# Optimization experiments

Hardware: AMD Instinct MI355X
Metric: run time of the kernel (lower is better)

## Reference

```python
import jax, jax.numpy as jnp
import numpy as np


def setup_inputs() -> dict:
    key = jax.random.key(0)
    k1, k2, k3 = jax.random.split(key, 3)
    bs, nvars, T, input_dim = 8, 16, 512, 256
    embed_dim, num_embed, codebook_num = 128, 512, 4
    inp = jax.random.normal(k1, (bs, nvars, T, input_dim), dtype=jnp.float32)
    # xavier_normal_ for (input_dim, embed_dim): std = sqrt(2/(fan_in+fan_out))
    xavier_std = float(np.sqrt(2.0 / (input_dim + embed_dim)))
    projector = jax.random.normal(k2, (input_dim, embed_dim), dtype=jnp.float32) * xavier_std
    codebook = jax.random.normal(k3, (codebook_num, num_embed, embed_dim), dtype=jnp.float32)
    return {"input": inp, "projector": projector, "codebook": codebook}


def reference(input, projector, codebook):
    # project: [b,n,t,input_dim] @ [input_dim,embed_dim] -> [b,n,t,d]
    x = jnp.matmul(input, projector)
    # L2-normalize along last dim (matches torch .norm(dim=-1,keepdim=True) division)
    x = x / jnp.linalg.norm(x, axis=-1, keepdims=True)
    cb = codebook / jnp.linalg.norm(codebook, axis=-1, keepdims=True)
    # cosine similarity: [b,n,t,c,m]
    similarity = jnp.einsum('bntd,cmd->bntcm', x, cb)
    # nearest code per codebook: [b,n,t,c]
    idx = jnp.argmax(similarity, axis=-1)
    return idx
```

## Files before the change

kernel.cpp:

```cpp
#include <hip/hip_runtime.h>
#include <math.h>

#define DIN    256
#define DEMB   128
#define NCB    4
#define MCODES 512
#define NCODE  2048
#define MARGIN 1.5e-4f

using bf16x8 = __attribute__((ext_vector_type(8))) short;
using f32x16 = __attribute__((ext_vector_type(16))) float;

static __device__ __forceinline__ unsigned short f2bf(float f) {
    unsigned u = __float_as_uint(f);
    u += 0x7FFFu + ((u >> 16) & 1u);
    return (unsigned short)(u >> 16);
}
static __device__ __forceinline__ float bf2f(unsigned short h) {
    return __uint_as_float(((unsigned)h) << 16);
}
static __device__ __forceinline__ float4 ld4(const float* p) {
    return *reinterpret_cast<const float4*>(p);
}
static __device__ __forceinline__ void gload_lds16(const void* g, void* l) {
    __builtin_amdgcn_global_load_lds(
        (const __attribute__((address_space(1))) void*)g,
        (__attribute__((address_space(3))) void*)l, 16, 0, 0);
}

__global__ __launch_bounds__(256) void prep_codebook(
        const float* __restrict__ cb, float* __restrict__ cbn,
        unsigned short* __restrict__ cbA) {
    const int w = threadIdx.x >> 6, lane = threadIdx.x & 63;
    const int code = blockIdx.x * 4 + w;
    const float2 v = reinterpret_cast<const float2*>(cb + (size_t)code * DEMB)[lane];
    float ss = v.x * v.x + v.y * v.y;
#pragma unroll
    for (int m = 1; m < 64; m <<= 1) ss += __shfl_xor(ss, m, 64);
    const float rn = 1.0f / sqrtf(ss);
    const float x0 = v.x * rn, x1 = v.y * rn;
    reinterpret_cast<float2*>(cbn + (size_t)code * DEMB)[lane] = make_float2(x0, x1);

    const unsigned short h0 = f2bf(x0), h1 = f2bf(x1);
    const unsigned short l0 = f2bf(x0 - bf2f(h0)), l1 = f2bf(x1 - bf2f(h1));
    const int ct = code >> 5, ci = code & 31;
    const int kt = lane >> 3, g = (lane >> 2) & 1, i = 2 * (lane & 3);
    const size_t base = ((size_t)ct * 1024 + kt * 128 + g * 32 + ci) * 8 + i;
    *reinterpret_cast<ushort2*>(cbA + base)       = make_ushort2(h0, h1);
    *reinterpret_cast<ushort2*>(cbA + base + 512) = make_ushort2(l0, l1);
}

__global__ __launch_bounds__(256) void prep_proj(
        const float* __restrict__ proj, unsigned short* __restrict__ pjA) {
    const int t = blockIdx.x * 256 + threadIdx.x;
    const int ci = t & 31, g = (t >> 5) & 1, kt = (t >> 6) & 15, mt = t >> 10;
    const int m = mt * 32 + ci;
    const size_t base = ((size_t)(mt * 16 + kt) * 3) * 512 + (size_t)(g * 32 + ci) * 8;
#pragma unroll
    for (int i = 0; i < 8; ++i) {
        const float v = proj[(size_t)(kt * 16 + g * 8 + i) * DEMB + m];
        const unsigned short h = f2bf(v);
        const float r1 = v - bf2f(h);
        const unsigned short md = f2bf(r1);
        const float r2 = r1 - bf2f(md);
        pjA[base + i]        = h;
        pjA[base + 512 + i]  = md;
        pjA[base + 1024 + i] = f2bf(r2);
    }
}

__global__ __launch_bounds__(256) void project_mfma(
        const float* __restrict__ inp, const unsigned short* __restrict__ pjA,
        float* __restrict__ xw, float* __restrict__ rnw) {
    const int tid = threadIdx.x;
    const int lane = tid & 63, wv = tid >> 6, kg = lane >> 5;
    const int row = blockIdx.x * 128 + wv * 32 + (lane & 31);
    const float* xr = inp + (size_t)row * DIN;
    const unsigned short* pL = pjA + (size_t)lane * 8;

    auto ldin = [&](float4& a, float4& b, int kt) {
        a = ld4(xr + kt * 16 + kg * 8);
        b = ld4(xr + kt * 16 + kg * 8 + 4);
    };

    f32x16 accP[4], accQ[4];
#pragma unroll
    for (int mt = 0; mt < 4; ++mt)
#pragma unroll
        for (int r = 0; r < 16; ++r) { accP[mt][r] = 0.0f; accQ[mt][r] = 0.0f; }

    auto do_step = [&](const float4& c0, const float4& c1, int kt) {
        const float xs[8] = {c0.x, c0.y, c0.z, c0.w, c1.x, c1.y, c1.z, c1.w};
        bf16x8 Bh, Bm, Bl;
#pragma unroll
        for (int e = 0; e < 8; ++e) {
            const float v = xs[e];
            const unsigned short h = f2bf(v);
            const float r1 = v - bf2f(h);
            const unsigned short md = f2bf(r1);
            const float r2 = r1 - bf2f(md);
            Bh[e] = (short)h; Bm[e] = (short)md; Bl[e] = (short)f2bf(r2);
        }
#pragma unroll
        for (int mt = 0; mt < 4; ++mt) {
            const unsigned short* pf = pL + ((size_t)(mt * 16 + kt) * 3) * 512;
            const bf16x8 Ah = *reinterpret_cast<const bf16x8*>(pf);
            const bf16x8 Am = *reinterpret_cast<const bf16x8*>(pf + 512);
            const bf16x8 Al = *reinterpret_cast<const bf16x8*>(pf + 1024);
            accP[mt] = __builtin_amdgcn_mfma_f32_32x32x16_bf16(Ah, Bh, accP[mt], 0, 0, 0);
            accQ[mt] = __builtin_amdgcn_mfma_f32_32x32x16_bf16(Ah, Bm, accQ[mt], 0, 0, 0);
            accQ[mt] = __builtin_amdgcn_mfma_f32_32x32x16_bf16(Am, Bh, accQ[mt], 0, 0, 0);
            accQ[mt] = __builtin_amdgcn_mfma_f32_32x32x16_bf16(Ah, Bl, accQ[mt], 0, 0, 0);
            accQ[mt] = __builtin_amdgcn_mfma_f32_32x32x16_bf16(Al, Bh, accQ[mt], 0, 0, 0);
            accQ[mt] = __builtin_amdgcn_mfma_f32_32x32x16_bf16(Am, Bm, accQ[mt], 0, 0, 0);
        }
    };

    float4 nA0, nA1, nB0, nB1;
    ldin(nA0, nA1, 0);
#pragma unroll 1
    for (int kt = 0; kt < 16; kt += 2) {
        ldin(nB0, nB1, kt + 1);
        do_step(nA0, nA1, kt);
        if (kt + 2 < 16) ldin(nA0, nA1, kt + 2);
        do_step(nB0, nB1, kt + 1);
    }

    float ss = 0.0f;
#pragma unroll
    for (int mt = 0; mt < 4; ++mt)
#pragma unroll
        for (int q = 0; q < 4; ++q) {
            float4 v;
            v.x = accP[mt][q * 4 + 0] + accQ[mt][q * 4 + 0];
            v.y = accP[mt][q * 4 + 1] + accQ[mt][q * 4 + 1];
            v.z = accP[mt][q * 4 + 2] + accQ[mt][q * 4 + 2];
            v.w = accP[mt][q * 4 + 3] + accQ[mt][q * 4 + 3];
            ss += v.x * v.x + v.y * v.y + v.z * v.z + v.w * v.w;
            *reinterpret_cast<float4*>(xw + (size_t)row * DEMB + mt * 32 + q * 8 + kg * 4) = v;
        }
    ss += __shfl_xor(ss, 32, 64);
    if (lane < 32) rnw[row] = 1.0f / sqrtf(ss);
}

__global__ __launch_bounds__(256) void project_kernel(
        const float* __restrict__ inp, const float* __restrict__ proj,
        float* __restrict__ xw, float* __restrict__ rnw) {
    const int tid = threadIdx.x, tx = tid & 31, ty = tid >> 5;
    const int rowBase = blockIdx.x * 64;

    float acc1[8][4];
#pragma unroll
    for (int i = 0; i < 8; ++i)
#pragma unroll
        for (int j = 0; j < 4; ++j) acc1[i][j] = 0.0f;

    const float* inRow0 = inp + (size_t)(rowBase + ty) * DIN;
    const float* pjCol  = proj + tx * 4;

    float4 ivA[8], ivB[8], pjA[4], pjB[4];
    auto load_step = [&](float4 iv[8], float4 pj[4], int kk) {
#pragma unroll
        for (int j = 0; j < 4; ++j) pj[j] = ld4(pjCol + (size_t)(kk + j) * DEMB);
#pragma unroll
        for (int i = 0; i < 8; ++i) iv[i] = ld4(inRow0 + (size_t)(8 * i) * DIN + kk);
    };
    auto fma_step = [&](const float4 iv[8], const float4 pj[4]) {
#pragma unroll
        for (int i = 0; i < 8; ++i) {
            const float* ivp = reinterpret_cast<const float*>(&iv[i]);
#pragma unroll
            for (int j = 0; j < 4; ++j) {
                acc1[i][0] = fmaf(ivp[j], pj[j].x, acc1[i][0]);
                acc1[i][1] = fmaf(ivp[j], pj[j].y, acc1[i][1]);
                acc1[i][2] = fmaf(ivp[j], pj[j].z, acc1[i][2]);
                acc1[i][3] = fmaf(ivp[j], pj[j].w, acc1[i][3]);
            }
        }
    };
    load_step(ivA, pjA, 0);
#pragma unroll 1
    for (int k = 0; k < DIN; k += 8) {
        load_step(ivB, pjB, k + 4);
        fma_step(ivA, pjA);
        if (k + 8 < DIN) load_step(ivA, pjA, k + 8);
        fma_step(ivB, pjB);
    }
#pragma unroll
    for (int i = 0; i < 8; ++i) {
        const int r = rowBase + ty + 8 * i;
        float ss = acc1[i][0] * acc1[i][0] + acc1[i][1] * acc1[i][1] +
                   acc1[i][2] * acc1[i][2] + acc1[i][3] * acc1[i][3];
#pragma unroll
        for (int mm = 1; mm < 32; mm <<= 1) ss += __shfl_xor(ss, mm, 64);
        if (tx == 0) rnw[r] = 1.0f / sqrtf(ss);
        *reinterpret_cast<float4*>(xw + (size_t)r * DEMB + tx * 4) =
            make_float4(acc1[i][0], acc1[i][1], acc1[i][2], acc1[i][3]);
    }
}

__global__ __launch_bounds__(256) void sim_kernel(
        const float* __restrict__ xw, const float* __restrict__ rnw,
        const unsigned short* __restrict__ cbA,
        int* __restrict__ out, int* __restrict__ unc_cnt,
        int* __restrict__ unc_list) {
    __shared__ __align__(16) short sA[3][8192];
    const int tid = threadIdx.x;
    const int lane = tid & 63, wv = tid >> 6;
    const int kg = lane >> 5;
    const int rowBase = blockIdx.x * 128;
    const int row = rowBase + wv * 32 + (lane & 31);

    auto stage = [&](int buf, int t) {
        const short* g = (const short*)cbA + (size_t)t * 8192 + wv * 2048 + lane * 8;
        short* l = &sA[buf][wv * 2048];
#pragma unroll
        for (int c = 0; c < 4; ++c)
            gload_lds16(g + c * 512, l + c * 512);
    };

    stage(0, 0);
    stage(1, 1);

    bf16x8 Bhi[8], Blo[8];
    {
        const float rn = rnw[row];
        const float* xr = xw + (size_t)row * DEMB;
#pragma unroll
        for (int kt = 0; kt < 8; ++kt) {
            const float4 f0 = ld4(xr + kt * 16 + kg * 8);
            const float4 f1 = ld4(xr + kt * 16 + kg * 8 + 4);
            const float xs[8] = {f0.x, f0.y, f0.z, f0.w, f1.x, f1.y, f1.z, f1.w};
            bf16x8 hv, lv;
#pragma unroll
            for (int e = 0; e < 8; ++e) {
                const float xn = xs[e] * rn;
                const unsigned short h = f2bf(xn);
                hv[e] = (short)h;
                lv[e] = (short)f2bf(xn - bf2f(h));
            }
            Bhi[kt] = hv; Blo[kt] = lv;
        }
    }

    f32x16 TWO, ZERO;
#pragma unroll
    for (int r = 0; r < 16; ++r) { TWO[r] = 2.0f; ZERO[r] = 0.0f; }

    f32x16 accA, accB1, accB2;
    float t1 = -INFINITY, t2 = -INFINITY; int i1 = 0;

    auto epi = [&](const f32x16& vA, const f32x16& vB1, const f32x16& vB2,
                   int gprev) {
        const int base = (gprev & 15) * 32;
#pragma unroll
        for (int r = 0; r < 16; ++r) {
            const float v = (vA[r] + vB1[r]) + vB2[r];
            const int gidx = base + (r & 3) + 8 * (r >> 2) + 4 * kg;
            t2 = fmaxf(t2, fminf(v, t1));
            if (v > t1) { t1 = v; i1 = gidx; }
        }
    };
    auto finalize = [&](int cb) {
        const float o1 = __shfl_xor(t1, 32, 64);
        const float o2 = __shfl_xor(t2, 32, 64);
        const int   oi = __shfl_xor(i1, 32, 64);
        const float m2 = fmaxf(fmaxf(t2, o2), fminf(t1, o1));
        if (o1 > t1 || (o1 == t1 && oi < i1)) { t1 = o1; i1 = oi; }
        const bool unc = (t1 - m2) < MARGIN;
        if (lane < 32 && !unc)
            out[(size_t)row * NCB + cb] = i1;
        unsigned long long msk = __ballot(unc && lane < 32);
        if (lane == 0 && msk) {
            const int n = __popcll(msk);
            int base = atomicAdd(unc_cnt, n);
            while (msk) {
                const int r = __ffsll(msk) - 1; msk &= msk - 1;
                unc_list[base++] = ((rowBase + wv * 32 + r) << 2) | cb;
            }
        }
        t1 = -INFINITY; t2 = -INFINITY; i1 = 0;
    };

#pragma unroll 1
    for (int g = 0; g < 64; ++g) {
        if (g < 63) asm volatile("s_waitcnt vmcnt(4)" ::: "memory");
        else        asm volatile("s_waitcnt vmcnt(0)" ::: "memory");
        __builtin_amdgcn_s_barrier();
        asm volatile("" ::: "memory");
        if (g + 2 < 64) stage((g + 2) % 3, g + 2);

        const short* pa = &sA[g % 3][lane * 8];
        f32x16 pA = accA, pB1 = accB1, pB2 = accB2;
        __builtin_amdgcn_s_setprio(1);
#pragma unroll
        for (int kt = 0; kt < 8; ++kt) {
            const bf16x8 Ahi = *reinterpret_cast<const bf16x8*>(pa + kt * 1024);
            const bf16x8 Alo = *reinterpret_cast<const bf16x8*>(pa + kt * 1024 + 512);
            accA  = __builtin_amdgcn_mfma_f32_32x32x16_bf16(Ahi, Bhi[kt], kt ? accA  : TWO,  0, 0, 0);
            accB1 = __builtin_amdgcn_mfma_f32_32x32x16_bf16(Ahi, Blo[kt], kt ? accB1 : ZERO, 0, 0, 0);
            accB2 = __builtin_amdgcn_mfma_f32_32x32x16_bf16(Alo, Bhi[kt], kt ? accB2 : ZERO, 0, 0, 0);
        }
        __builtin_amdgcn_s_setprio(0);

        if (g > 0) {
            epi(pA, pB1, pB2, g - 1);
            if ((g & 15) == 0) finalize((g >> 4) - 1);
        }
    }
    epi(accA, accB1, accB2, 63);
    finalize(3);
}

__global__ __launch_bounds__(256) void recheck_kernel(
        const float* __restrict__ inp, const float* __restrict__ proj,
        const float* __restrict__ cbn,
        const int* __restrict__ unc_cnt, const int* __restrict__ unc_list,
        int* __restrict__ out) {
    __shared__ float sx[4][DEMB];
    const int lane = threadIdx.x & 63, wv = threadIdx.x >> 6;
    const int n = *unc_cnt;
    for (int it = blockIdx.x * 4 + wv; it < n; it += gridDim.x * 4) {
        const int item = unc_list[it];
        const int row = item >> 2, cbi = item & 3;
        {
            const float* ir = inp + (size_t)row * DIN;
            float a0 = 0.0f, a1 = 0.0f;
#pragma unroll 2
            for (int k = 0; k < DIN; k += 4) {
                const float4 iv = ld4(ir + k);
                const float* ivp = reinterpret_cast<const float*>(&iv);
#pragma unroll
                for (int j = 0; j < 4; ++j) {
                    a0 = fmaf(ivp[j], proj[(size_t)(k + j) * DEMB + lane],      a0);
                    a1 = fmaf(ivp[j], proj[(size_t)(k + j) * DEMB + lane + 64], a1);
                }
            }
            sx[wv][lane] = a0; sx[wv][lane + 64] = a1;
        }
        float best = -INFINITY; int bi = 0;
#pragma unroll 2
        for (int j = 0; j < 8; ++j) {
            const int c = lane + 64 * j;
            const float* cv = cbn + ((size_t)cbi * MCODES + c) * DEMB;
            float s0 = 0, s1 = 0, s2 = 0, s3 = 0;
#pragma unroll 4
            for (int k = 0; k < DEMB; k += 4) {
                const float4 xk = ld4(&sx[wv][k]);
                const float4 ck = ld4(cv + k);
                s0 = fmaf(xk.x, ck.x, s0); s1 = fmaf(xk.y, ck.y, s1);
                s2 = fmaf(xk.z, ck.z, s2); s3 = fmaf(xk.w, ck.w, s3);
            }
            const float s = (s0 + s1) + (s2 + s3);
            if (s > best) { best = s; bi = c; }
        }
#pragma unroll
        for (int mm = 1; mm < 64; mm <<= 1) {
            const float ov = __shfl_xor(best, mm, 64);
            const int   oc = __shfl_xor(bi, mm, 64);
            if (ov > best || (ov == best && oc < bi)) { best = ov; bi = oc; }
        }
        if (lane == 0) out[(size_t)row * NCB + cbi] = bi;
    }
}

__global__ __launch_bounds__(256) void fused_quantize_kernel(
        const float* __restrict__ inp, const float* __restrict__ proj,
        const float* __restrict__ cbn, const unsigned short* __restrict__ cbA,
        int* __restrict__ out) {
    __shared__ float sX[128][132];
    __shared__ float sRn[128];
    const int tid = threadIdx.x;
    const int tx = tid & 31, ty = tid >> 5;
    const int rowBase = blockIdx.x * 128;

#pragma unroll 1
    for (int p = 0; p < 2; ++p) {
        float acc1[8][4];
#pragma unroll
        for (int i = 0; i < 8; ++i)
#pragma unroll
            for (int j = 0; j < 4; ++j) acc1[i][j] = 0.0f;
        const float* inRow0 = inp + (size_t)(rowBase + p * 64 + ty) * DIN;
        const float* pjCol  = proj + tx * 4;
        float4 ivA[8], ivB[8], pjA[4], pjB[4];
        auto load_step = [&](float4 iv[8], float4 pj[4], int kk) {
#pragma unroll
            for (int j = 0; j < 4; ++j) pj[j] = ld4(pjCol + (size_t)(kk + j) * DEMB);
#pragma unroll
            for (int i = 0; i < 8; ++i) iv[i] = ld4(inRow0 + (size_t)(8 * i) * DIN + kk);
        };
        auto fma_step = [&](const float4 iv[8], const float4 pj[4]) {
#pragma unroll
            for (int i = 0; i < 8; ++i) {
                const float* ivp = reinterpret_cast<const float*>(&iv[i]);
#pragma unroll
                for (int j = 0; j < 4; ++j) {
                    acc1[i][0] = fmaf(ivp[j], pj[j].x, acc1[i][0]);
                    acc1[i][1] = fmaf(ivp[j], pj[j].y, acc1[i][1]);
                    acc1[i][2] = fmaf(ivp[j], pj[j].z, acc1[i][2]);
                    acc1[i][3] = fmaf(ivp[j], pj[j].w, acc1[i][3]);
                }
            }
        };
        load_step(ivA, pjA, 0);
#pragma unroll 1
        for (int k = 0; k < DIN; k += 8) {
            load_step(ivB, pjB, k + 4);
            fma_step(ivA, pjA);
            if (k + 8 < DIN) load_step(ivA, pjA, k + 8);
            fma_step(ivB, pjB);
        }
#pragma unroll
        for (int i = 0; i < 8; ++i) {
            const int r = p * 64 + ty + 8 * i;
            float ss = acc1[i][0] * acc1[i][0] + acc1[i][1] * acc1[i][1] +
                       acc1[i][2] * acc1[i][2] + acc1[i][3] * acc1[i][3];
#pragma unroll
            for (int mm = 1; mm < 32; mm <<= 1) ss += __shfl_xor(ss, mm, 64);
            if (tx == 0) sRn[r] = 1.0f / sqrtf(ss);
            *reinterpret_cast<float4*>(&sX[r][tx * 4]) =
                make_float4(acc1[i][0], acc1[i][1], acc1[i][2], acc1[i][3]);
        }
    }
    __syncthreads();

    const int lane = tid & 63, wv = tid >> 6;
    const int kg = lane >> 5;
    const int rowL = wv * 32 + (lane & 31);
    bf16x8 Bhi[8], Blo[8];
    {
        const float rn = sRn[rowL];
#pragma unroll
        for (int kt = 0; kt < 8; ++kt) {
            const int k0 = kt * 16 + kg * 8;
            float4 f0 = ld4(&sX[rowL][k0]);
            float4 f1 = ld4(&sX[rowL][k0 + 4]);
            float xs[8] = {f0.x, f0.y, f0.z, f0.w, f1.x, f1.y, f1.z, f1.w};
            bf16x8 hv, lv;
#pragma unroll
            for (int e = 0; e < 8; ++e) {
                const float xn = xs[e] * rn;
                const unsigned short h = f2bf(xn);
                hv[e] = (short)h;
                lv[e] = (short)f2bf(xn - bf2f(h));
            }
            Bhi[kt] = hv; Blo[kt] = lv;
        }
    }
    float t1 = -INFINITY, t2 = -INFINITY; int i1 = 0;
    const short* pA = reinterpret_cast<const short*>(cbA) + (size_t)lane * 8;
#pragma unroll 1
    for (int ct = 0; ct < 64; ++ct) {
        if ((ct & 1) == 0) __syncthreads();
        const short* pct = pA + (size_t)ct * 8192;
        f32x16 accA, accB;
#pragma unroll
        for (int r = 0; r < 16; ++r) { accA[r] = 0.0f; accB[r] = 0.0f; }
#pragma unroll
        for (int kt = 0; kt < 8; ++kt) {
            const bf16x8 Ahi = *reinterpret_cast<const bf16x8*>(pct + kt * 1024);
            const bf16x8 Alo = *reinterpret_cast<const bf16x8*>(pct + kt * 1024 + 512);
            accA = __builtin_amdgcn_mfma_f32_32x32x16_bf16(Ahi, Bhi[kt], accA, 0, 0, 0);
            accB = __builtin_amdgcn_mfma_f32_32x32x16_bf16(Ahi, Blo[kt], accB, 0, 0, 0);
            accB = __builtin_amdgcn_mfma_f32_32x32x16_bf16(Alo, Bhi[kt], accB, 0, 0, 0);
        }
#pragma unroll
        for (int r = 0; r < 16; ++r) {
            const float v = accA[r] + accB[r];
            const int gidx = ct * 32 + ((r & 3) + 8 * (r >> 2) + 4 * kg);
            t2 = fmaxf(t2, fminf(v, t1));
            if (v > t1) { t1 = v; i1 = gidx; }
        }
        if ((ct & 15) == 15) {
            const int cbi = ct >> 4;
            const float o1 = __shfl_xor(t1, 32, 64);
            const float o2 = __shfl_xor(t2, 32, 64);
            const int   oi = __shfl_xor(i1, 32, 64);
            const float m2 = fmaxf(fmaxf(t2, o2), fminf(t1, o1));
            if (o1 > t1 || (o1 == t1 && oi < i1)) { t1 = o1; i1 = oi; }
            const bool unc = (t1 - m2) < MARGIN;
            if (lane < 32 && !unc)
                out[(size_t)(rowBase + rowL) * NCB + cbi] = i1 - cbi * MCODES;
            unsigned long long msk = __ballot(unc && lane < 32);
            while (msk) {
                const int r = __ffsll(msk) - 1; msk &= msk - 1;
                const int rl = wv * 32 + r;
                float best = -INFINITY; int bi = 0;
#pragma unroll 1
                for (int j = 0; j < 8; ++j) {
                    const int c = lane + 64 * j;
                    const float* cv = cbn + ((size_t)cbi * MCODES + c) * DEMB;
                    float s0 = 0, s1 = 0, s2 = 0, s3 = 0;
#pragma unroll
                    for (int k = 0; k < DEMB; k += 4) {
                        const float4 xk = ld4(&sX[rl][k]);
                        const float4 ck = ld4(cv + k);
                        s0 = fmaf(xk.x, ck.x, s0); s1 = fmaf(xk.y, ck.y, s1);
                        s2 = fmaf(xk.z, ck.z, s2); s3 = fmaf(xk.w, ck.w, s3);
                    }
                    const float s = (s0 + s1) + (s2 + s3);
                    if (s > best) { best = s; bi = c; }
                }
#pragma unroll
                for (int mm = 1; mm < 64; mm <<= 1) {
                    const float ov = __shfl_xor(best, mm, 64);
                    const int   oc = __shfl_xor(bi, mm, 64);
                    if (ov > best || (ov == best && oc < bi)) { best = ov; bi = oc; }
                }
                if (lane == 0) out[(size_t)(rowBase + rl) * NCB + cbi] = bi;
            }
            t1 = -INFINITY; t2 = -INFINITY; i1 = 0;
        }
    }
}

extern "C" void kernel_launch(void* const* d_in, const int* in_sizes, int n_in,
                              void* d_out, int out_size, void* d_ws, size_t ws_size,
                              hipStream_t stream) {
    const float* inp  = (const float*)d_in[0];
    const float* proj = (const float*)d_in[1];
    const float* cb   = (const float*)d_in[2];
    int* out = (int*)d_out;

    char* ws = (char*)d_ws;
    float* cbn = (float*)ws;
    unsigned short* cbA = (unsigned short*)(ws + (1 << 20));
    float* rnw = (float*)(ws + (2 << 20));
    float* xw  = (float*)(ws + (2 << 20) + (1 << 18));
    const size_t off_cnt = (size_t)(2 << 20) + (1 << 18) + ((size_t)32 << 20);
    int* unc_cnt  = (int*)(ws + off_cnt);
    int* unc_list = (int*)(ws + off_cnt + 256);
    const size_t off_pjA = off_cnt + 256 + (1 << 20);
    unsigned short* pjA = (unsigned short*)(ws + off_pjA);
    const size_t need_old = off_pjA;
    const size_t need_new = off_pjA + 192 * 1024;

    hipLaunchKernelGGL(prep_codebook, dim3(NCODE / 4), dim3(256), 0, stream,
                       cb, cbn, cbA);
    if (ws_size >= need_old) {
        hipMemsetAsync(unc_cnt, 0, 4, stream);
        if (ws_size >= need_new) {
            hipLaunchKernelGGL(prep_proj, dim3(16), dim3(256), 0, stream, proj, pjA);
            hipLaunchKernelGGL(project_mfma, dim3(512), dim3(256), 0, stream,
                               inp, pjA, xw, rnw);
        } else {
            hipLaunchKernelGGL(project_kernel, dim3(1024), dim3(256), 0, stream,
                               inp, proj, xw, rnw);
        }
        hipLaunchKernelGGL(sim_kernel, dim3(512), dim3(256), 0, stream,
                           xw, rnw, cbA, out, unc_cnt, unc_list);
        hipLaunchKernelGGL(recheck_kernel, dim3(1024), dim3(256), 0, stream,
                           inp, proj, cbn, unc_cnt, unc_list, out);
    } else {
        hipLaunchKernelGGL(fused_quantize_kernel, dim3(512), dim3(256), 0, stream,
                           inp, proj, cbn, cbA, out);
    }
}
```

Baseline: 238.1 us.

## Split projection and similarity kernels across output tiles and codebooks for more parallelism

The projection kernel now gives each wave one 32-column output tile instead of all four, with a 4x larger grid. The similarity kernel assigns one codebook per block, also with a 4x larger grid, and computes the row norm itself from xw, which removes the rnw buffer. The three separate MFMA accumulators are merged into a single chained accumulator. This raises occupancy and lowers register pressure, at the cost of reading the input rows and xw redundantly across blocks and serialising the MFMA dependency chain.

```diff
diff --git a/kernel.cpp b/kernel.cpp
--- a/kernel.cpp
+++ b/kernel.cpp
@@ -71,10 +71,10 @@
 
 __global__ __launch_bounds__(256) void project_mfma(
         const float* __restrict__ inp, const unsigned short* __restrict__ pjA,
-        float* __restrict__ xw, float* __restrict__ rnw) {
+        float* __restrict__ xw) {
     const int tid = threadIdx.x;
-    const int lane = tid & 63, wv = tid >> 6, kg = lane >> 5;
-    const int row = blockIdx.x * 128 + wv * 32 + (lane & 31);
+    const int lane = tid & 63, mt = tid >> 6, kg = lane >> 5;
+    const int row = blockIdx.x * 32 + (lane & 31);
     const float* xr = inp + (size_t)row * DIN;
     const unsigned short* pL = pjA + (size_t)lane * 8;
 
@@ -83,11 +83,9 @@
         b = ld4(xr + kt * 16 + kg * 8 + 4);
     };
 
-    f32x16 accP[4], accQ[4];
-#pragma unroll
-    for (int mt = 0; mt < 4; ++mt)
-#pragma unroll
-        for (int r = 0; r < 16; ++r) { accP[mt][r] = 0.0f; accQ[mt][r] = 0.0f; }
+    f32x16 P, Q;
+#pragma unroll
+    for (int r = 0; r < 16; ++r) { P[r] = 0.0f; Q[r] = 0.0f; }
 
     auto do_step = [&](const float4& c0, const float4& c1, int kt) {
         const float xs[8] = {c0.x, c0.y, c0.z, c0.w, c1.x, c1.y, c1.z, c1.w};
@@ -101,19 +99,16 @@
             const float r2 = r1 - bf2f(md);
             Bh[e] = (short)h; Bm[e] = (short)md; Bl[e] = (short)f2bf(r2);
         }
-#pragma unroll
-        for (int mt = 0; mt < 4; ++mt) {
-            const unsigned short* pf = pL + ((size_t)(mt * 16 + kt) * 3) * 512;
-            const bf16x8 Ah = *reinterpret_cast<const bf16x8*>(pf);
-            const bf16x8 Am = *reinterpret_cast<const bf16x8*>(pf + 512);
-            const bf16x8 Al = *reinterpret_cast<const bf16x8*>(pf + 1024);
-            accP[mt] = __builtin_amdgcn_mfma_f32_32x32x16_bf16(Ah, Bh, accP[mt], 0, 0, 0);
-            accQ[mt] = __builtin_amdgcn_mfma_f32_32x32x16_bf16(Ah, Bm, accQ[mt], 0, 0, 0);
-            accQ[mt] = __builtin_amdgcn_mfma_f32_32x32x16_bf16(Am, Bh, accQ[mt], 0, 0, 0);
-            accQ[mt] = __builtin_amdgcn_mfma_f32_32x32x16_bf16(Ah, Bl, accQ[mt], 0, 0, 0);
-            accQ[mt] = __builtin_amdgcn_mfma_f32_32x32x16_bf16(Al, Bh, accQ[mt], 0, 0, 0);
-            accQ[mt] = __builtin_amdgcn_mfma_f32_32x32x16_bf16(Am, Bm, accQ[mt], 0, 0, 0);
-        }
+        const unsigned short* pf = pL + ((size_t)(mt * 16 + kt) * 3) * 512;
+        const bf16x8 Ah = *reinterpret_cast<const bf16x8*>(pf);
+        const bf16x8 Am = *reinterpret_cast<const bf16x8*>(pf + 512);
+        const bf16x8 Al = *reinterpret_cast<const bf16x8*>(pf + 1024);
+        P = __builtin_amdgcn_mfma_f32_32x32x16_bf16(Ah, Bh, P, 0, 0, 0);
+        Q = __builtin_amdgcn_mfma_f32_32x32x16_bf16(Ah, Bm, Q, 0, 0, 0);
+        Q = __builtin_amdgcn_mfma_f32_32x32x16_bf16(Am, Bh, Q, 0, 0, 0);
+        Q = __builtin_amdgcn_mfma_f32_32x32x16_bf16(Ah, Bl, Q, 0, 0, 0);
+        Q = __builtin_amdgcn_mfma_f32_32x32x16_bf16(Al, Bh, Q, 0, 0, 0);
+        Q = __builtin_amdgcn_mfma_f32_32x32x16_bf16(Am, Bm, Q, 0, 0, 0);
     };
 
     float4 nA0, nA1, nB0, nB1;
@@ -126,26 +121,20 @@
         do_step(nB0, nB1, kt + 1);
     }
 
-    float ss = 0.0f;
-#pragma unroll
-    for (int mt = 0; mt < 4; ++mt)
-#pragma unroll
-        for (int q = 0; q < 4; ++q) {
-            float4 v;
-            v.x = accP[mt][q * 4 + 0] + accQ[mt][q * 4 + 0];
-            v.y = accP[mt][q * 4 + 1] + accQ[mt][q * 4 + 1];
-            v.z = accP[mt][q * 4 + 2] + accQ[mt][q * 4 + 2];
-            v.w = accP[mt][q * 4 + 3] + accQ[mt][q * 4 + 3];
-            ss += v.x * v.x + v.y * v.y + v.z * v.z + v.w * v.w;
-            *reinterpret_cast<float4*>(xw + (size_t)row * DEMB + mt * 32 + q * 8 + kg * 4) = v;
-        }
-    ss += __shfl_xor(ss, 32, 64);
-    if (lane < 32) rnw[row] = 1.0f / sqrtf(ss);
+#pragma unroll
+    for (int q = 0; q < 4; ++q) {
+        float4 v;
+        v.x = P[q * 4 + 0] + Q[q * 4 + 0];
+        v.y = P[q * 4 + 1] + Q[q * 4 + 1];
+        v.z = P[q * 4 + 2] + Q[q * 4 + 2];
+        v.w = P[q * 4 + 3] + Q[q * 4 + 3];
+        *reinterpret_cast<float4*>(xw + (size_t)row * DEMB + mt * 32 + q * 8 + kg * 4) = v;
+    }
 }
 
 __global__ __launch_bounds__(256) void project_kernel(
         const float* __restrict__ inp, const float* __restrict__ proj,
-        float* __restrict__ xw, float* __restrict__ rnw) {
+        float* __restrict__ xw) {
     const int tid = threadIdx.x, tx = tid & 31, ty = tid >> 5;
     const int rowBase = blockIdx.x * 64;
 
@@ -189,18 +178,13 @@
 #pragma unroll
     for (int i = 0; i < 8; ++i) {
         const int r = rowBase + ty + 8 * i;
-        float ss = acc1[i][0] * acc1[i][0] + acc1[i][1] * acc1[i][1] +
-                   acc1[i][2] * acc1[i][2] + acc1[i][3] * acc1[i][3];
-#pragma unroll
-        for (int mm = 1; mm < 32; mm <<= 1) ss += __shfl_xor(ss, mm, 64);
-        if (tx == 0) rnw[r] = 1.0f / sqrtf(ss);
         *reinterpret_cast<float4*>(xw + (size_t)r * DEMB + tx * 4) =
             make_float4(acc1[i][0], acc1[i][1], acc1[i][2], acc1[i][3]);
     }
 }
 
 __global__ __launch_bounds__(256) void sim_kernel(
-        const float* __restrict__ xw, const float* __restrict__ rnw,
+        const float* __restrict__ xw,
         const unsigned short* __restrict__ cbA,
         int* __restrict__ out, int* __restrict__ unc_cnt,
         int* __restrict__ unc_list) {
@@ -208,11 +192,13 @@
     const int tid = threadIdx.x;
     const int lane = tid & 63, wv = tid >> 6;
     const int kg = lane >> 5;
-    const int rowBase = blockIdx.x * 128;
+    const int cbi = blockIdx.x & 3;
+    const int rowBase = (blockIdx.x >> 2) * 128;
     const int row = rowBase + wv * 32 + (lane & 31);
 
+    const short* gA = (const short*)cbA + (size_t)cbi * 16 * 8192;
     auto stage = [&](int buf, int t) {
-        const short* g = (const short*)cbA + (size_t)t * 8192 + wv * 2048 + lane * 8;
+        const short* g = gA + (size_t)t * 8192 + wv * 2048 + lane * 8;
         short* l = &sA[buf][wv * 2048];
 #pragma unroll
         for (int c = 0; c < 4; ++c)
@@ -224,13 +210,24 @@
 
     bf16x8 Bhi[8], Blo[8];
     {
-        const float rn = rnw[row];
         const float* xr = xw + (size_t)row * DEMB;
+        float4 f0[8], f1[8];
+        float ss = 0.0f;
 #pragma unroll
         for (int kt = 0; kt < 8; ++kt) {
-            const float4 f0 = ld4(xr + kt * 16 + kg * 8);
-            const float4 f1 = ld4(xr + kt * 16 + kg * 8 + 4);
-            const float xs[8] = {f0.x, f0.y, f0.z, f0.w, f1.x, f1.y, f1.z, f1.w};
+            f0[kt] = ld4(xr + kt * 16 + kg * 8);
+            f1[kt] = ld4(xr + kt * 16 + kg * 8 + 4);
+            ss += f0[kt].x * f0[kt].x + f0[kt].y * f0[kt].y +
+                  f0[kt].z * f0[kt].z + f0[kt].w * f0[kt].w +
+                  f1[kt].x * f1[kt].x + f1[kt].y * f1[kt].y +
+                  f1[kt].z * f1[kt].z + f1[kt].w * f1[kt].w;
+        }
+        ss += __shfl_xor(ss, 32, 64);
+        const float rn = 1.0f / sqrtf(ss);
+#pragma unroll
+        for (int kt = 0; kt < 8; ++kt) {
+            const float xs[8] = {f0[kt].x, f0[kt].y, f0[kt].z, f0[kt].w,
+                                 f1[kt].x, f1[kt].y, f1[kt].z, f1[kt].w};
             bf16x8 hv, lv;
 #pragma unroll
             for (int e = 0; e < 8; ++e) {
@@ -243,73 +240,74 @@
         }
     }
 
-    f32x16 TWO, ZERO;
-#pragma unroll
-    for (int r = 0; r < 16; ++r) { TWO[r] = 2.0f; ZERO[r] = 0.0f; }
-
-    f32x16 accA, accB1, accB2;
+    f32x16 TWO;
+#pragma unroll
+    for (int r = 0; r < 16; ++r) TWO[r] = 2.0f;
+
+    f32x16 acc = TWO;
     float t1 = -INFINITY, t2 = -INFINITY; int i1 = 0;
 
-    auto epi = [&](const f32x16& vA, const f32x16& vB1, const f32x16& vB2,
-                   int gprev) {
-        const int base = (gprev & 15) * 32;
+#pragma unroll 1
+    for (int g = 0; g < 16; ++g) {
+        if (g < 15) asm volatile("s_waitcnt vmcnt(4)" ::: "memory");
+        else        asm volatile("s_waitcnt vmcnt(0)" ::: "memory");
+        __builtin_amdgcn_s_barrier();
+        asm volatile("" ::: "memory");
+        if (g + 2 < 16) stage((g + 2) % 3, g + 2);
+
+        const short* pa = &sA[g % 3][lane * 8];
+        const f32x16 pAcc = acc;
+        __builtin_amdgcn_s_setprio(1);
+#pragma unroll
+        for (int kt = 0; kt < 8; ++kt) {
+            const bf16x8 Ahi = *reinterpret_cast<const bf16x8*>(pa + kt * 1024);
+            const bf16x8 Alo = *reinterpret_cast<const bf16x8*>(pa + kt * 1024 + 512);
+            acc = __builtin_amdgcn_mfma_f32_32x32x16_bf16(Ahi, Bhi[kt], kt ? acc : TWO, 0, 0, 0);
+            acc = __builtin_amdgcn_mfma_f32_32x32x16_bf16(Ahi, Blo[kt], acc, 0, 0, 0);
+            acc = __builtin_amdgcn_mfma_f32_32x32x16_bf16(Alo, Bhi[kt], acc, 0, 0, 0);
+        }
+        __builtin_amdgcn_s_setprio(0);
+
+        if (g > 0) {
+            const int base = (g - 1) * 32;
+#pragma unroll
+            for (int r = 0; r < 16; ++r) {
+                const float v = pAcc[r];
+                const int gidx = base + (r & 3) + 8 * (r >> 2) + 4 * kg;
+                t2 = fmaxf(t2, fminf(v, t1));
+                if (v > t1) { t1 = v; i1 = gidx; }
+            }
+        }
+    }
+    {
+        const int base = 15 * 32;
 #pragma unroll
         for (int r = 0; r < 16; ++r) {
-            const float v = (vA[r] + vB1[r]) + vB2[r];
+            const float v = acc[r];
             const int gidx = base + (r & 3) + 8 * (r >> 2) + 4 * kg;
             t2 = fmaxf(t2, fminf(v, t1));
             if (v > t1) { t1 = v; i1 = gidx; }
         }
-    };
-    auto finalize = [&](int cb) {
-        const float o1 = __shfl_xor(t1, 32, 64);
-        const float o2 = __shfl_xor(t2, 32, 64);
-        const int   oi = __shfl_xor(i1, 32, 64);
-        const float m2 = fmaxf(fmaxf(t2, o2), fminf(t1, o1));
-        if (o1 > t1 || (o1 == t1 && oi < i1)) { t1 = o1; i1 = oi; }
-        const bool unc = (t1 - m2) < MARGIN;
-        if (lane < 32 && !unc)
-            out[(size_t)row * NCB + cb] = i1;
-        unsigned long long msk = __ballot(unc && lane < 32);
-        if (lane == 0 && msk) {
-            const int n = __popcll(msk);
-            int base = atomicAdd(unc_cnt, n);
-            while (msk) {
-                const int r = __ffsll(msk) - 1; msk &= msk - 1;
-                unc_list[base++] = ((rowBase + wv * 32 + r) << 2) | cb;
-            }
-        }
-        t1 = -INFINITY; t2 = -INFINITY; i1 = 0;
-    };
-
-#pragma unroll 1
-    for (int g = 0; g < 64; ++g) {
-        if (g < 63) asm volatile("s_waitcnt vmcnt(4)" ::: "memory");
-        else        asm volatile("s_waitcnt vmcnt(0)" ::: "memory");
-        __builtin_amdgcn_s_barrier();
-        asm volatile("" ::: "memory");
-        if (g + 2 < 64) stage((g + 2) % 3, g + 2);
-
-        const short* pa = &sA[g % 3][lane * 8];
-        f32x16 pA = accA, pB1 = accB1, pB2 = accB2;
-        __builtin_amdgcn_s_setprio(1);
-#pragma unroll
-        for (int kt = 0; kt < 8; ++kt) {
-            const bf16x8 Ahi = *reinterpret_cast<const bf16x8*>(pa + kt * 1024);
-            const bf16x8 Alo = *reinterpret_cast<const bf16x8*>(pa + kt * 1024 + 512);
-            accA  = __builtin_amdgcn_mfma_f32_32x32x16_bf16(Ahi, Bhi[kt], kt ? accA  : TWO,  0, 0, 0);
-            accB1 = __builtin_amdgcn_mfma_f32_32x32x16_bf16(Ahi, Blo[kt], kt ? accB1 : ZERO, 0, 0, 0);
-            accB2 = __builtin_amdgcn_mfma_f32_32x32x16_bf16(Alo, Bhi[kt], kt ? accB2 : ZERO, 0, 0, 0);
-        }
-        __builtin_amdgcn_s_setprio(0);
-
-        if (g > 0) {
-            epi(pA, pB1, pB2, g - 1);
-            if ((g & 15) == 0) finalize((g >> 4) - 1);
-        }
-    }
-    epi(accA, accB1, accB2, 63);
-    finalize(3);
+    }
+
+    const float o1 = __shfl_xor(t1, 32, 64);
+    const float o2 = __shfl_xor(t2, 32, 64);
+    const int   oi = __shfl_xor(i1, 32, 64);
+    const float m2 = fmaxf(fmaxf(t2, o2), fminf(t1, o1));
+    if (o1 > t1 || (o1 == t1 && oi < i1)) { t1 = o1; i1 = oi; }
+    const bool unc = (t1 - m2) < MARGIN;
+    if (lane < 32 && !unc)
+        out[(size_t)row * NCB + cbi] = i1;
+
+    unsigned long long msk = __ballot(unc && lane < 32);
+    if (lane == 0 && msk) {
+        const int n = __popcll(msk);
+        int base = atomicAdd(unc_cnt, n);
+        while (msk) {
+            const int r = __ffsll(msk) - 1; msk &= msk - 1;
+            unc_list[base++] = ((rowBase + wv * 32 + r) << 2) | cbi;
+        }
+    }
 }
 
 __global__ __launch_bounds__(256) void recheck_kernel(
@@ -526,7 +524,6 @@
     char* ws = (char*)d_ws;
     float* cbn = (float*)ws;
     unsigned short* cbA = (unsigned short*)(ws + (1 << 20));
-    float* rnw = (float*)(ws + (2 << 20));
     float* xw  = (float*)(ws + (2 << 20) + (1 << 18));
     const size_t off_cnt = (size_t)(2 << 20) + (1 << 18) + ((size_t)32 << 20);
     int* unc_cnt  = (int*)(ws + off_cnt);
@@ -542,14 +539,14 @@
         hipMemsetAsync(unc_cnt, 0, 4, stream);
         if (ws_size >= need_new) {
             hipLaunchKernelGGL(prep_proj, dim3(16), dim3(256), 0, stream, proj, pjA);
-            hipLaunchKernelGGL(project_mfma, dim3(512), dim3(256), 0, stream,
-                               inp, pjA, xw, rnw);
+            hipLaunchKernelGGL(project_mfma, dim3(2048), dim3(256), 0, stream,
+                               inp, pjA, xw);
         } else {
             hipLaunchKernelGGL(project_kernel, dim3(1024), dim3(256), 0, stream,
-                               inp, proj, xw, rnw);
-        }
-        hipLaunchKernelGGL(sim_kernel, dim3(512), dim3(256), 0, stream,
-                           xw, rnw, cbA, out, unc_cnt, unc_list);
+                               inp, proj, xw);
+        }
+        hipLaunchKernelGGL(sim_kernel, dim3(2048), dim3(256), 0, stream,
+                           xw, cbA, out, unc_cnt, unc_list);
         hipLaunchKernelGGL(recheck_kernel, dim3(1024), dim3(256), 0, stream,
                            inp, proj, cbn, unc_cnt, unc_list, out);
     } else {
```

Result: no change. 234.8 us (-1.4%).
